# Optimization experiments

Measured on AMD Instinct MI355X. Metric: run time of the kernel, lower is better.

Reference implementation:

```python
import jax, jax.numpy as jnp
import numpy as np

EMBED = 256
HEADS = 8
SR = 2
RED = 2


def setup_inputs() -> dict:
    key = jax.random.key(0)
    ks = jax.random.split(key, 12)
    N, B, C = 1024, 64, EMBED
    inp = {
        "query": jax.random.normal(ks[0], (N, B, C), jnp.float32),
        "H": 32,
        "W": 32,
        "key": jax.random.normal(ks[1], (N, B, C), jnp.float32),
        "value": jax.random.normal(ks[2], (N, B, C), jnp.float32),
        # parameters
        "in_proj_weight": jax.random.normal(ks[3], (3 * C, C), jnp.float32) * (1.0 / np.sqrt(C)),
        "in_proj_bias": jnp.zeros((3 * C,), jnp.float32),
        "sr_w": jax.random.normal(ks[4], (C, C, SR, SR), jnp.float32) * np.sqrt(2.0 / (SR * SR * C)),
        "sr_b": jnp.zeros((C,), jnp.float32),
        "norm_g": jnp.ones((C,), jnp.float32),
        "norm_b": jnp.zeros((C,), jnp.float32),
        "out_w": jax.random.normal(ks[5], (C, C), jnp.float32) * (1.0 / np.sqrt(C)),
        "out_b": jnp.zeros((C,), jnp.float32),
        "se_w1": jax.random.normal(ks[6], (C // RED, C), jnp.float32) * 0.02,
        "se_w2": jax.random.normal(ks[7], (C, C // RED), jnp.float32) * 0.02,
    }
    return inp


def _angles(H, W):
    # get_index: a = (pi/2)*(i//W)/H, b = (pi/2)*(i%W)/W for flattened row-major index
    c = np.pi / 2
    idx = jnp.arange(H * W)
    a = c * (idx // W).astype(jnp.float32) / H
    b = c * (idx % W).astype(jnp.float32) / W
    return a, b


def _layernorm(x, g, b, eps=1e-5):
    mu = jnp.mean(x, -1, keepdims=True)
    var = jnp.mean(jnp.square(x - mu), -1, keepdims=True)
    return (x - mu) * jax.lax.rsqrt(var + eps) * g + b


def _abs_clamp(t, lo=1e-4, hi=1e4):
    return jnp.clip(jnp.abs(t), lo, hi) * jnp.sign(t)


def reference(query, H, W, key, value, in_proj_weight, in_proj_bias, sr_w, sr_b,
              norm_g, norm_b, out_w, out_b, se_w1, se_w2):
    N, B, C = query.shape
    h = HEADS
    hd = C // h
    scaling = hd ** (-0.5)

    x = jnp.transpose(query, (1, 0, 2))  # (B, N, C)

    # squeeze-excite gate from query: mean over tokens -> fc1 -> relu -> fc2 -> sigmoid
    se = jnp.mean(x, axis=1)                       # (B, C)
    se = jax.nn.sigmoid(jax.nn.relu(se @ se_w1.T) @ se_w2.T)  # (B, C)

    # spatial reduction conv (kernel=stride=sr_ratio) + layernorm for k/v source
    x_img = jnp.transpose(x, (0, 2, 1)).reshape(B, C, H, W)
    xr = jax.lax.conv_general_dilated(
        x_img, sr_w, window_strides=(SR, SR), padding="VALID",
        dimension_numbers=("NCHW", "OIHW", "NCHW"))
    xr = xr + sr_b[None, :, None, None]
    Hs, Ws = H // SR, W // SR
    Ns = Hs * Ws
    xr = jnp.transpose(xr.reshape(B, C, Ns), (0, 2, 1))  # (B, Ns, C)
    xr = _layernorm(xr, norm_g, norm_b)

    Wq, Wk, Wv = in_proj_weight[:C], in_proj_weight[C:2 * C], in_proj_weight[2 * C:]
    bq, bk, bv = in_proj_bias[:C], in_proj_bias[C:2 * C], in_proj_bias[2 * C:]

    def split_heads(t):  # (B, L, C) -> (B*h, L, hd)
        Bb, L, _ = t.shape
        return jnp.transpose(t.reshape(Bb, L, h, hd), (0, 2, 1, 3)).reshape(Bb * h, L, hd)

    q = split_heads((x @ Wq.T + bq) * scaling)
    k = split_heads(xr @ Wk.T + bk)
    v = split_heads(xr @ Wv.T + bv)

    q = jax.nn.relu(q)
    k = jax.nn.relu(k)

    # cosFormer-2d "sum" reweighting: cos(a_i - a_j) + cos(b_i - b_j)
    a, b = _angles(H, W)       # (N,)
    a2, b2 = _angles(Hs, Ws)   # (Ns,)

    def reweight(t, aa, bb):  # (BH, L, hd), angles (L,) -> (BH, L, 4*hd)
        aa = aa[None, :, None]
        bb = bb[None, :, None]
        return jnp.concatenate(
            [t * jnp.cos(aa), t * jnp.sin(aa), t * jnp.cos(bb), t * jnp.sin(bb)], axis=-1)

    q_ = reweight(q, a, b)     # (BH, N, 4hd)
    k_ = reweight(k, a2, b2)   # (BH, Ns, 4hd)

    # linear attention: never materialize the NxNs matrix
    kv = jnp.einsum("bnd,bnm->bdm", k_, v)             # (BH, 4hd, hd)
    denom = jnp.einsum("bnd,bd->bn", q_, k_.sum(1))    # (BH, N)
    denom = _abs_clamp(denom)
    attn = jnp.einsum("bnd,bdm->bnm", q_, kv) / denom[..., None]  # (BH, N, hd)

    attn = jnp.transpose(attn.reshape(B, h, N, hd), (0, 2, 1, 3)).reshape(B, N, C)
    out = attn @ out_w.T + out_b            # (B, N, C)
    out = out * se[:, None, :]              # SE channel gating
    return jnp.transpose(out, (1, 0, 2))    # (N, B, C)
```

## Files before the change

kernel.cpp:

```cpp
#include <hip/hip_runtime.h>

#define NTOK 1024
#define NB   64
#define CD   256
#define NHEAD 8
#define HDIM 32
#define NS 256
#define NBC 16384

typedef __attribute__((ext_vector_type(8))) short short8v;
typedef __attribute__((ext_vector_type(4))) short short4v;
typedef __attribute__((ext_vector_type(4))) float f32x4;

__device__ __forceinline__ unsigned bfr(float x){
  unsigned u = __float_as_uint(x);
  return (u + 0x7fffu + ((u>>16)&1u)) >> 16;
}
__device__ __forceinline__ void split2(float x, short &h, short &l){
  unsigned hu = bfr(x);
  float hf = __uint_as_float(hu << 16);
  unsigned lu = bfr(x - hf);
  h = (short)hu; l = (short)lu;
}

__global__ __launch_bounds__(256) void k_wcvt(const float* __restrict__ ipw, const float* __restrict__ ow,
                                              const float* __restrict__ srw,
                                              short* __restrict__ Wih, short* __restrict__ Wil,
                                              short* __restrict__ Woh, short* __restrict__ Wol,
                                              short* __restrict__ Wsh, short* __restrict__ Wsl){
  int u = blockIdx.x*256 + threadIdx.x;
  float xs[8];
  short* dh; short* dl; int dof;
  if (u < 24576){
    int n = u >> 5, off = (u & 31)*8;
    const float* s = ipw + n*CD + off;
    #pragma unroll
    for (int i=0;i<8;++i) xs[i] = s[i];
    dh = Wih; dl = Wil; dof = n*CD + off;
  } else if (u < 32768){
    int v = u - 24576;
    int n = v >> 5, off = (v & 31)*8;
    const float* s = ow + n*CD + off;
    #pragma unroll
    for (int i=0;i<8;++i) xs[i] = s[i];
    dh = Woh; dl = Wol; dof = n*CD + off;
  } else {
    int v = u - 32768;
    int n = v >> 7, koff = (v & 127)*8;
    int g = koff >> 8, cin0 = koff & 255;
    #pragma unroll
    for (int i=0;i<8;++i) xs[i] = srw[n*1024 + (cin0+i)*4 + g];
    dh = Wsh; dl = Wsl; dof = n*1024 + koff;
  }
  short8v h, l;
  #pragma unroll
  for (int i=0;i<8;++i){ short a,b; split2(xs[i],a,b); h[i]=a; l[i]=b; }
  *(short8v*)(dh + dof) = h;
  *(short8v*)(dl + dof) = l;
}

__global__ __launch_bounds__(256) void k_qcvt(const float* __restrict__ q, short* __restrict__ Qh,
                                              short* __restrict__ Ql){
  int idx = blockIdx.x*256 + threadIdx.x;
  int m = idx >> 5;
  int off = (idx & 31)*8;
  const float* src = q + (m & 1023)*NBC + (m >> 10)*CD + off;
  float4 a = *(const float4*)src;
  float4 b4 = *(const float4*)(src+4);
  float xs[8] = {a.x,a.y,a.z,a.w,b4.x,b4.y,b4.z,b4.w};
  short8v h, l;
  #pragma unroll
  for (int i=0;i<8;++i){ short hh,ll; split2(xs[i],hh,ll); h[i]=hh; l[i]=ll; }
  *(short8v*)(Qh + m*CD + off) = h;
  *(short8v*)(Ql + m*CD + off) = l;
}

__global__ __launch_bounds__(256) void k_trig(float* __restrict__ t1, float* __restrict__ t2){
  int n = blockIdx.x*256 + threadIdx.x;
  const float c = 1.57079632679489662f;
  float aa = c * (float)(n >> 5) / 32.0f;
  float bb = c * (float)(n & 31) / 32.0f;
  t1[n*4+0]=cosf(aa); t1[n*4+1]=sinf(aa); t1[n*4+2]=cosf(bb); t1[n*4+3]=sinf(bb);
  if (n < 256){
    float a2 = c * (float)(n >> 4) / 16.0f;
    float b2 = c * (float)(n & 15) / 16.0f;
    t2[n*4+0]=cosf(a2); t2[n*4+1]=sinf(a2); t2[n*4+2]=cosf(b2); t2[n*4+3]=sinf(b2);
  }
}

__global__ __launch_bounds__(256) void k_semean(const float* __restrict__ q, float* __restrict__ part){
  int b = blockIdx.x >> 2, qr = blockIdx.x & 3;
  int c = threadIdx.x;
  const float* qp = q + (qr*256)*NBC + b*CD + c;
  float s0=0.f,s1=0.f,s2=0.f,s3=0.f;
  for (int n=0;n<256;n+=4){
    s0 += qp[(n  )*NBC];
    s1 += qp[(n+1)*NBC];
    s2 += qp[(n+2)*NBC];
    s3 += qp[(n+3)*NBC];
  }
  part[blockIdx.x*256 + c] = (s0+s1)+(s2+s3);
}

__global__ __launch_bounds__(256) void k_semlp(const float* __restrict__ part, const float* __restrict__ w1,
                                               const float* __restrict__ w2, float* __restrict__ se){
  __shared__ float sm[256];
  __shared__ float s1s[128];
  int b = blockIdx.x, t = threadIdx.x;
  float s = (part[(b*4+0)*256+t]+part[(b*4+1)*256+t])+(part[(b*4+2)*256+t]+part[(b*4+3)*256+t]);
  sm[t] = s*(1.0f/1024.0f);
  __syncthreads();
  if (t < 128){
    float a = 0.f;
    const float* wr = w1 + t*256;
    for (int c=0;c<256;c+=4){
      float4 wf = *(const float4*)(wr+c);
      a += sm[c]*wf.x + sm[c+1]*wf.y + sm[c+2]*wf.z + sm[c+3]*wf.w;
    }
    s1s[t] = fmaxf(a, 0.f);
  }
  __syncthreads();
  float a = 0.f;
  const float* wr2 = w2 + t*128;
  for (int c=0;c<128;c+=4){
    float4 wf = *(const float4*)(wr2+c);
    a += s1s[c]*wf.x + s1s[c+1]*wf.y + s1s[c+2]*wf.z + s1s[c+3]*wf.w;
  }
  se[b*256+t] = 1.0f/(1.0f+expf(-a));
}

__global__ __launch_bounds__(256) void k_conv(const short* __restrict__ Qh, const short* __restrict__ Ql,
                                              const short* __restrict__ Wsh, const short* __restrict__ Wsl,
                                              const float* __restrict__ srb, float* __restrict__ xr){
  __shared__ __align__(16) short Ah[64*32];
  __shared__ __align__(16) short Al[64*32];
  __shared__ __align__(16) short Bh[128*32];
  __shared__ __align__(16) short Bl[128*32];
  int mblk = blockIdx.x >> 1, nblk = blockIdx.x & 1;
  int m0 = mblk*64, n0 = nblk*128;
  int b = mblk >> 2;
  int pos0 = m0 & 255;
  int t = threadIdx.x, wave = t>>6, lane = t&63;
  int wm = wave>>1, wn = wave&1;
  int q = lane>>4, r = lane&15;
  int ra = t>>2, pa = (t&3)*8;
  int posA = pos0 + ra, hs = posA>>4, ws2 = posA&15;
  const f32x4 fz = {0.f,0.f,0.f,0.f};
  f32x4 acc[2][4];
  #pragma unroll
  for (int s=0;s<2;++s)
    #pragma unroll
    for (int tt=0;tt<4;++tt) acc[s][tt] = fz;
  for (int kc=0; kc<32; ++kc){
    int g = kc>>3, cin0 = (kc&7)*32;
    int gh = g>>1, gw = g&1;
    int tok = (2*hs+gh)*32 + 2*ws2 + gw;
    int ga = ((b<<10) + tok)*CD + cin0 + pa;
    *(short8v*)(Ah + ra*32 + pa) = *(const short8v*)(Qh + ga);
    *(short8v*)(Al + ra*32 + pa) = *(const short8v*)(Ql + ga);
    int ko = kc*32;
    #pragma unroll
    for (int rep=0; rep<2; ++rep){
      int rr = ra + rep*64;
      int gb = (n0 + rr)*1024 + ko + pa;
      *(short8v*)(Bh + rr*32 + pa) = *(const short8v*)(Wsh + gb);
      *(short8v*)(Bl + rr*32 + pa) = *(const short8v*)(Wsl + gb);
    }
    __syncthreads();
    short8v ah[2], al[2];
    #pragma unroll
    for (int s=0;s<2;++s){
      int row = wm*32 + s*16 + r;
      ah[s] = *(const short8v*)(Ah + row*32 + q*8);
      al[s] = *(const short8v*)(Al + row*32 + q*8);
    }
    #pragma unroll
    for (int tt=0;tt<4;++tt){
      int brow = wn*64 + tt*16 + r;
      short8v bh = *(const short8v*)(Bh + brow*32 + q*8);
      short8v bl = *(const short8v*)(Bl + brow*32 + q*8);
      #pragma unroll
      for (int s=0;s<2;++s){
        acc[s][tt] = __builtin_amdgcn_mfma_f32_16x16x32_bf16(ah[s], bh, acc[s][tt], 0,0,0);
        acc[s][tt] = __builtin_amdgcn_mfma_f32_16x16x32_bf16(ah[s], bl, acc[s][tt], 0,0,0);
        acc[s][tt] = __builtin_amdgcn_mfma_f32_16x16x32_bf16(al[s], bh, acc[s][tt], 0,0,0);
      }
    }
    __syncthreads();
  }
  #pragma unroll
  for (int s=0;s<2;++s){
    #pragma unroll
    for (int tt=0;tt<4;++tt){
      int c = n0 + wn*64 + tt*16 + r;
      float bias = srb[c];
      #pragma unroll
      for (int i=0;i<4;++i){
        int m = m0 + wm*32 + s*16 + q*4 + i;
        xr[m*CD + c] = acc[s][tt][i] + bias;
      }
    }
  }
}

__global__ __launch_bounds__(256) void k_ln(const float* __restrict__ xr, const float* __restrict__ g,
                                            const float* __restrict__ bta, short* __restrict__ Xh,
                                            short* __restrict__ Xl){
  int wv = threadIdx.x >> 6, lane = threadIdx.x & 63;
  int row = blockIdx.x*4 + wv;
  float4 v = ((const float4*)(xr + row*CD))[lane];
  float s = (v.x+v.y)+(v.z+v.w);
  #pragma unroll
  for (int off=1; off<64; off<<=1) s += __shfl_xor(s, off, 64);
  float mu = s * (1.0f/256.0f);
  float dx=v.x-mu, dy=v.y-mu, dz=v.z-mu, dw=v.w-mu;
  float s2 = (dx*dx+dy*dy)+(dz*dz+dw*dw);
  #pragma unroll
  for (int off=1; off<64; off<<=1) s2 += __shfl_xor(s2, off, 64);
  float inv = 1.0f / sqrtf(s2*(1.0f/256.0f) + 1e-5f);
  float4 gr = ((const float4*)g)[lane];
  float4 br = ((const float4*)bta)[lane];
  float o0 = dx*inv*gr.x + br.x;
  float o1 = dy*inv*gr.y + br.y;
  float o2 = dz*inv*gr.z + br.z;
  float o3 = dw*inv*gr.w + br.w;
  short4v h, l; short a0,b0;
  split2(o0,a0,b0); h[0]=a0; l[0]=b0;
  split2(o1,a0,b0); h[1]=a0; l[1]=b0;
  split2(o2,a0,b0); h[2]=a0; l[2]=b0;
  split2(o3,a0,b0); h[3]=a0; l[3]=b0;
  *(short4v*)(Xh + row*CD + lane*4) = h;
  *(short4v*)(Xl + row*CD + lane*4) = l;
}

__global__ __launch_bounds__(256) void k_qproj(const short* __restrict__ Qh, const short* __restrict__ Ql,
                                               const short* __restrict__ Wih, const short* __restrict__ Wil,
                                               const float* __restrict__ ipb,
                                               short* __restrict__ Qbh, short* __restrict__ Qbl){
  __shared__ __align__(16) short smem[16384];
  short* Ah = smem;
  short* Al = smem + 4096;
  short* Bh = smem + 8192;
  short* Bl = smem + 12288;
  int mblk = blockIdx.x >> 1, nblk = blockIdx.x & 1;
  int m0 = mblk*128, n0 = nblk*128;
  int t = threadIdx.x, wave = t>>6, lane = t&63;
  int wm = wave>>1, wn = wave&1;
  int q = lane>>4, r = lane&15;
  int cr = t>>2, cp = (t&3)*8;
  int cpS = (((t&3) ^ ((cr>>1)&3)))*8;
  int sw8 = ((r>>1)&3)*8;
  const f32x4 fz = {0.f,0.f,0.f,0.f};
  f32x4 acc[4][4];
  #pragma unroll
  for (int s=0;s<4;++s)
    #pragma unroll
    for (int tt=0;tt<4;++tt) acc[s][tt] = fz;
  for (int kc=0; kc<8; ++kc){
    int ko = kc*32;
    #pragma unroll
    for (int rep=0; rep<2; ++rep){
      int rr = cr + rep*64;
      int ga = (m0 + rr)*CD + ko + cp;
      *(short8v*)(Ah + rr*32 + cpS) = *(const short8v*)(Qh + ga);
      *(short8v*)(Al + rr*32 + cpS) = *(const short8v*)(Ql + ga);
      int gb = (n0 + rr)*CD + ko + cp;
      *(short8v*)(Bh + rr*32 + cpS) = *(const short8v*)(Wih + gb);
      *(short8v*)(Bl + rr*32 + cpS) = *(const short8v*)(Wil + gb);
    }
    __syncthreads();
    short8v ah[4], al[4];
    #pragma unroll
    for (int s=0;s<4;++s){
      int row = wm*64 + s*16 + r;
      ah[s] = *(const short8v*)(Ah + row*32 + ((q*8)^sw8));
      al[s] = *(const short8v*)(Al + row*32 + ((q*8)^sw8));
    }
    #pragma unroll
    for (int tt=0;tt<4;++tt){
      int brow = wn*64 + tt*16 + r;
      short8v bh = *(const short8v*)(Bh + brow*32 + ((q*8)^sw8));
      short8v bl = *(const short8v*)(Bl + brow*32 + ((q*8)^sw8));
      #pragma unroll
      for (int s=0;s<4;++s){
        acc[s][tt] = __builtin_amdgcn_mfma_f32_16x16x32_bf16(ah[s], bh, acc[s][tt], 0,0,0);
        acc[s][tt] = __builtin_amdgcn_mfma_f32_16x16x32_bf16(ah[s], bl, acc[s][tt], 0,0,0);
        acc[s][tt] = __builtin_amdgcn_mfma_f32_16x16x32_bf16(al[s], bh, acc[s][tt], 0,0,0);
      }
    }
    __syncthreads();
  }
  const float sc = 0.17677669529663687f;
  short* T = smem;
  #pragma unroll
  for (int s=0;s<4;++s){
    #pragma unroll
    for (int tt=0;tt<4;++tt){
      int c_loc = wn*64 + tt*16 + r;
      int chunk = c_loc >> 3, cb = c_loc & 7;
      float bias = ipb[n0 + c_loc];
      #pragma unroll
      for (int i=0;i<4;++i){
        int m_loc = wm*64 + s*16 + q*4 + i;
        float val = fmaxf(acc[s][tt][i] + bias, 0.f)*sc;
        unsigned hu = bfr(val);
        T[m_loc*128 + ((chunk ^ (m_loc&7))<<3) + cb] = (short)hu;
        acc[s][tt][i] = val - __uint_as_float(hu<<16);
      }
    }
  }
  __syncthreads();
  {
    int mrl = (lane>>2);
    int ccl = lane&3;
    #pragma unroll
    for (int e=0;e<8;++e){
      int hl = e&3, mg = e>>2;
      int m_loc = wave*32 + mg*16 + mrl;
      int cc16 = hl*4 + ccl;
      short8v v = *(const short8v*)(T + m_loc*128 + ((cc16 ^ (m_loc&7))<<3));
      *(short8v*)(Qbh + ((size_t)((n0>>5)+hl))*2097152 + (size_t)(m0+m_loc)*32 + ccl*8) = v;
    }
  }
  __syncthreads();
  #pragma unroll
  for (int s=0;s<4;++s){
    #pragma unroll
    for (int tt=0;tt<4;++tt){
      int c_loc = wn*64 + tt*16 + r;
      int chunk = c_loc >> 3, cb = c_loc & 7;
      #pragma unroll
      for (int i=0;i<4;++i){
        int m_loc = wm*64 + s*16 + q*4 + i;
        T[m_loc*128 + ((chunk ^ (m_loc&7))<<3) + cb] = (short)bfr(acc[s][tt][i]);
      }
    }
  }
  __syncthreads();
  {
    int mrl = (lane>>2);
    int ccl = lane&3;
    #pragma unroll
    for (int e=0;e<8;++e){
      int hl = e&3, mg = e>>2;
      int m_loc = wave*32 + mg*16 + mrl;
      int cc16 = hl*4 + ccl;
      short8v v = *(const short8v*)(T + m_loc*128 + ((cc16 ^ (m_loc&7))<<3));
      *(short8v*)(Qbl + ((size_t)((n0>>5)+hl))*2097152 + (size_t)(m0+m_loc)*32 + ccl*8) = v;
    }
  }
}

__global__ __launch_bounds__(256) void k_kvproj(const short* __restrict__ Xh, const short* __restrict__ Xl,
                                                const short* __restrict__ Wkh, const short* __restrict__ Wkl,
                                                const float* __restrict__ ipb, float* __restrict__ kb,
                                                float* __restrict__ vb){
  __shared__ __align__(16) short Ah[128*32];
  __shared__ __align__(16) short Al[128*32];
  __shared__ __align__(16) short Bh[128*32];
  __shared__ __align__(16) short Bl[128*32];
  int mblk = blockIdx.x >> 2, nblk = blockIdx.x & 3;
  int m0 = mblk*128, n0 = nblk*128;
  int t = threadIdx.x, wave = t>>6, lane = t&63;
  int wm = wave>>1, wn = wave&1;
  int q = lane>>4, r = lane&15;
  int cr = t>>2, cp = (t&3)*8;
  const f32x4 fz = {0.f,0.f,0.f,0.f};
  f32x4 acc[4][4];
  #pragma unroll
  for (int s=0;s<4;++s)
    #pragma unroll
    for (int tt=0;tt<4;++tt) acc[s][tt] = fz;
  for (int kc=0; kc<8; ++kc){
    int ko = kc*32;
    #pragma unroll
    for (int rep=0; rep<2; ++rep){
      int rr = cr + rep*64;
      int ga = (m0 + rr)*CD + ko + cp;
      *(short8v*)(Ah + rr*32 + cp) = *(const short8v*)(Xh + ga);
      *(short8v*)(Al + rr*32 + cp) = *(const short8v*)(Xl + ga);
      int gb = (n0 + rr)*CD + ko + cp;
      *(short8v*)(Bh + rr*32 + cp) = *(const short8v*)(Wkh + gb);
      *(short8v*)(Bl + rr*32 + cp) = *(const short8v*)(Wkl + gb);
    }
    __syncthreads();
    short8v ah[4], al[4];
    #pragma unroll
    for (int s=0;s<4;++s){
      int row = wm*64 + s*16 + r;
      ah[s] = *(const short8v*)(Ah + row*32 + q*8);
      al[s] = *(const short8v*)(Al + row*32 + q*8);
    }
    #pragma unroll
    for (int tt=0;tt<4;++tt){
      int brow = wn*64 + tt*16 + r;
      short8v bh = *(const short8v*)(Bh + brow*32 + q*8);
      short8v bl = *(const short8v*)(Bl + brow*32 + q*8);
      #pragma unroll
      for (int s=0;s<4;++s){
        acc[s][tt] = __builtin_amdgcn_mfma_f32_16x16x32_bf16(ah[s], bh, acc[s][tt], 0,0,0);
        acc[s][tt] = __builtin_amdgcn_mfma_f32_16x16x32_bf16(ah[s], bl, acc[s][tt], 0,0,0);
        acc[s][tt] = __builtin_amdgcn_mfma_f32_16x16x32_bf16(al[s], bh, acc[s][tt], 0,0,0);
      }
    }
    __syncthreads();
  }
  #pragma unroll
  for (int s=0;s<4;++s){
    #pragma unroll
    for (int tt=0;tt<4;++tt){
      int c = n0 + wn*64 + tt*16 + r;
      float bias = ipb[256 + c];
      #pragma unroll
      for (int i=0;i<4;++i){
        int m = m0 + wm*64 + s*16 + q*4 + i;
        float v = acc[s][tt][i] + bias;
        if (c < 256) kb[m*CD + c] = fmaxf(v, 0.f);
        else         vb[m*CD + (c-256)] = v;
      }
    }
  }
}

__global__ __launch_bounds__(256) void k_kv(const float* __restrict__ kb, const float* __restrict__ vbuf,
                                            const float* __restrict__ t2, short* __restrict__ Bhp,
                                            short* __restrict__ Blp){
  int bh = blockIdx.x; int b = bh >> 3, h = bh & 7;
  int t = threadIdx.x; int jq = t >> 5, m = t & 31;
  float acc[4][4];
  #pragma unroll
  for (int p=0;p<4;++p){ acc[p][0]=0.f; acc[p][1]=0.f; acc[p][2]=0.f; acc[p][3]=0.f; }
  const float* kbase = kb + h*HDIM + jq*4;
  const float* vbase = vbuf + h*HDIM + m;
  for (int n=0;n<256;++n){
    int ro = (b*NS + n)*CD;
    float4 k4 = *(const float4*)(kbase + ro);
    float vv = vbase[ro];
    float4 tt = *(const float4*)(t2 + n*4);
    float tv[4] = {tt.x, tt.y, tt.z, tt.w};
    float kk[4] = {k4.x, k4.y, k4.z, k4.w};
    #pragma unroll
    for (int p=0;p<4;++p){
      float tp = tv[p]*vv;
      #pragma unroll
      for (int jj=0;jj<4;++jj) acc[p][jj] += tp*kk[jj];
    }
  }
  short* bhb = Bhp + bh*4608;
  short* blb = Blp + bh*4608;
  #pragma unroll
  for (int p=0;p<4;++p){
    short4v h4, l4;
    #pragma unroll
    for (int jj=0;jj<4;++jj){ short a,bq; split2(acc[p][jj],a,bq); h4[jj]=a; l4[jj]=bq; }
    *(short4v*)(bhb + (p*32+m)*32 + jq*4) = h4;
    *(short4v*)(blb + (p*32+m)*32 + jq*4) = l4;
  }
  if (t < 128){
    int p = t >> 5, j = t & 31;
    float s=0.f;
    const float* kp = kb + h*HDIM + j;
    for (int n=0;n<256;++n) s += t2[n*4+p]*kp[(b*NS+n)*CD];
    short a,bq; split2(s,a,bq);
    bhb[(128+p)*32 + j] = a;
    blb[(128+p)*32 + j] = bq;
  } else {
    int idx = t - 128;
    #pragma unroll
    for (int ii=0;ii<3;++ii){
      bhb[4224 + idx*3 + ii] = 0;
      blb[4224 + idx*3 + ii] = 0;
    }
  }
}

__global__ __launch_bounds__(256) void k_attn(const short* __restrict__ Qbh, const short* __restrict__ Qbl,
                                              const short* __restrict__ Bhg, const short* __restrict__ Blg,
                                              const float* __restrict__ t1,
                                              short* __restrict__ Ath, short* __restrict__ Atl){
  __shared__ __align__(16) short Bh[144*32];
  __shared__ __align__(16) short Bl[144*32];
  __shared__ __align__(16) short Ah[256*32];
  __shared__ __align__(16) short Al[256*32];
  int bh = blockIdx.x, b = bh>>3, h = bh&7;
  int t = threadIdx.x, lane = t&63, wave = t>>6;
  int q = lane>>4, r = lane&15;
  {
    const short8v* sh = (const short8v*)(Bhg + bh*4608);
    const short8v* sl = (const short8v*)(Blg + bh*4608);
    for (int i=t; i<576; i+=256){
      ((short8v*)Bh)[i] = sh[i];
      ((short8v*)Bl)[i] = sl[i];
    }
  }
  __syncthreads();
  short8v bf_h[9], bf_l[9];
  #pragma unroll
  for (int nt=0; nt<9; ++nt){
    int row = nt*16 + r;
    bf_h[nt] = *(const short8v*)(Bh + row*32 + q*8);
    bf_l[nt] = *(const short8v*)(Bl + row*32 + q*8);
  }
  const short* qh_base = Qbh + ((size_t)h*65536 + (size_t)b*1024)*32;
  const short* ql_base = Qbl + ((size_t)h*65536 + (size_t)b*1024)*32;
  const f32x4 fz = {0.f,0.f,0.f,0.f};
  for (int u=0; u<4; ++u){
    __syncthreads();
    {
      const short8v* sh = (const short8v*)(qh_base + (u*256 + t)*32);
      const short8v* sl = (const short8v*)(ql_base + (u*256 + t)*32);
      short8v* dh = (short8v*)(Ah + t*32);
      short8v* dl = (short8v*)(Al + t*32);
      #pragma unroll
      for (int i=0;i<4;++i){ dh[i]=sh[i]; dl[i]=sl[i]; }
    }
    __syncthreads();
    #pragma unroll
    for (int mi=0; mi<4; ++mi){
      int mt = wave*4 + mi;
      short8v ah = *(const short8v*)(Ah + (mt*16 + r)*32 + q*8);
      short8v al = *(const short8v*)(Al + (mt*16 + r)*32 + q*8);
      f32x4 acc[9];
      #pragma unroll
      for (int nt=0;nt<9;++nt) acc[nt]=fz;
      #pragma unroll
      for (int nt=0;nt<9;++nt){
        acc[nt] = __builtin_amdgcn_mfma_f32_16x16x32_bf16(ah, bf_h[nt], acc[nt],0,0,0);
        acc[nt] = __builtin_amdgcn_mfma_f32_16x16x32_bf16(ah, bf_l[nt], acc[nt],0,0,0);
        acc[nt] = __builtin_amdgcn_mfma_f32_16x16x32_bf16(al, bf_h[nt], acc[nt],0,0,0);
      }
      int nbase = u*256 + mt*16 + q*4;
      int src = lane & 48;
      #pragma unroll
      for (int i=0;i<4;++i){
        int n = nbase + i;
        float4 tv = *(const float4*)(t1 + n*4);
        float dp0 = __shfl(acc[8][i], src+0, 64);
        float dp1 = __shfl(acc[8][i], src+1, 64);
        float dp2 = __shfl(acc[8][i], src+2, 64);
        float dp3 = __shfl(acc[8][i], src+3, 64);
        float den = tv.x*dp0 + tv.y*dp1 + tv.z*dp2 + tv.w*dp3;
        float a0 = tv.x*acc[0][i] + tv.y*acc[2][i] + tv.z*acc[4][i] + tv.w*acc[6][i];
        float a1 = tv.x*acc[1][i] + tv.y*acc[3][i] + tv.z*acc[5][i] + tv.w*acc[7][i];
        float sgn = (den>0.f) ? 1.f : ((den<0.f)? -1.f : 0.f);
        float ad = fminf(fmaxf(fabsf(den), 1e-4f), 1e4f);
        float inv = (den != 0.f) ? 1.0f/(ad*sgn) : 0.f;
        float o0 = a0*inv, o1 = a1*inv;
        int mrow = b*NTOK + n;
        short h0,l0,h1,l1;
        split2(o0,h0,l0); split2(o1,h1,l1);
        Ath[mrow*CD + h*HDIM + r]      = h0;
        Atl[mrow*CD + h*HDIM + r]      = l0;
        Ath[mrow*CD + h*HDIM + 16 + r] = h1;
        Atl[mrow*CD + h*HDIM + 16 + r] = l1;
      }
    }
  }
}

__global__ __launch_bounds__(256) void k_outproj(const short* __restrict__ Ath, const short* __restrict__ Atl,
                                                 const short* __restrict__ Woh, const short* __restrict__ Wol,
                                                 const float* __restrict__ obv, const float* __restrict__ se,
                                                 float* __restrict__ dout){
  __shared__ __align__(16) short Ah[128*32];
  __shared__ __align__(16) short Al[128*32];
  __shared__ __align__(16) short Bh[128*32];
  __shared__ __align__(16) short Bl[128*32];
  int mblk = blockIdx.x >> 1, nblk = blockIdx.x & 1;
  int m0 = mblk*128, n0 = nblk*128;
  int t = threadIdx.x, wave = t>>6, lane = t&63;
  int wm = wave>>1, wn = wave&1;
  int q = lane>>4, r = lane&15;
  int cr = t>>2, cp = (t&3)*8;
  const f32x4 fz = {0.f,0.f,0.f,0.f};
  f32x4 acc[4][4];
  #pragma unroll
  for (int s=0;s<4;++s)
    #pragma unroll
    for (int tt=0;tt<4;++tt) acc[s][tt] = fz;
  for (int kc=0; kc<8; ++kc){
    int ko = kc*32;
    #pragma unroll
    for (int rep=0; rep<2; ++rep){
      int rr = cr + rep*64;
      int ga = (m0 + rr)*CD + ko + cp;
      *(short8v*)(Ah + rr*32 + cp) = *(const short8v*)(Ath + ga);
      *(short8v*)(Al + rr*32 + cp) = *(const short8v*)(Atl + ga);
      int gb = (n0 + rr)*CD + ko + cp;
      *(short8v*)(Bh + rr*32 + cp) = *(const short8v*)(Woh + gb);
      *(short8v*)(Bl + rr*32 + cp) = *(const short8v*)(Wol + gb);
    }
    __syncthreads();
    short8v ah[4], al[4];
    #pragma unroll
    for (int s=0;s<4;++s){
      int row = wm*64 + s*16 + r;
      ah[s] = *(const short8v*)(Ah + row*32 + q*8);
      al[s] = *(const short8v*)(Al + row*32 + q*8);
    }
    #pragma unroll
    for (int tt=0;tt<4;++tt){
      int brow = wn*64 + tt*16 + r;
      short8v bh = *(const short8v*)(Bh + brow*32 + q*8);
      short8v bl = *(const short8v*)(Bl + brow*32 + q*8);
      #pragma unroll
      for (int s=0;s<4;++s){
        acc[s][tt] = __builtin_amdgcn_mfma_f32_16x16x32_bf16(ah[s], bh, acc[s][tt], 0,0,0);
        acc[s][tt] = __builtin_amdgcn_mfma_f32_16x16x32_bf16(ah[s], bl, acc[s][tt], 0,0,0);
        acc[s][tt] = __builtin_amdgcn_mfma_f32_16x16x32_bf16(al[s], bh, acc[s][tt], 0,0,0);
      }
    }
    __syncthreads();
  }
  #pragma unroll
  for (int s=0;s<4;++s){
    #pragma unroll
    for (int tt=0;tt<4;++tt){
      int c = n0 + wn*64 + tt*16 + r;
      float bias = obv[c];
      #pragma unroll
      for (int i=0;i<4;++i){
        int m = m0 + wm*64 + s*16 + q*4 + i;
        int bb = m >> 10, ntok = m & 1023;
        float sev = se[bb*CD + c];
        dout[(ntok*NB + bb)*CD + c] = (acc[s][tt][i] + bias)*sev;
      }
    }
  }
}

extern "C" void kernel_launch(void* const* d_in, const int* in_sizes, int n_in,
                              void* d_out, int out_size, void* d_ws, size_t ws_size,
                              hipStream_t stream) {
  const float* query = (const float*)d_in[0];
  const float* ipw = (const float*)d_in[5];
  const float* ipb = (const float*)d_in[6];
  const float* srw = (const float*)d_in[7];
  const float* srb = (const float*)d_in[8];
  const float* ng  = (const float*)d_in[9];
  const float* nbb = (const float*)d_in[10];
  const float* ow  = (const float*)d_in[11];
  const float* obv = (const float*)d_in[12];
  const float* sw1 = (const float*)d_in[13];
  const float* sw2 = (const float*)d_in[14];
  float* dout = (float*)d_out;
  float* ws = (float*)d_ws;

  short* Qbh  = (short*)ws;
  short* Qbl  = (short*)(ws + 8388608);
  float* R1   = ws + 16777216;
  short* Qh   = (short*)R1;
  short* Ql   = (short*)(R1 + 8388608);
  float* kb   = R1;
  float* vb   = R1 + 4194304;
  short* Ath  = (short*)R1;
  short* Atl  = (short*)(R1 + 8388608);
  float* xr   = ws + 33554432;
  short* Xh   = (short*)(ws + 37748736);
  short* Xl   = (short*)(ws + 39845888);
  short* kvbh = (short*)(ws + 41943040);
  short* kvbl = (short*)(ws + 43122688);
  float* part = ws + 44302336;
  float* se   = ws + 44367872;
  float* t1   = ws + 44384256;
  float* t2   = ws + 44388352;
  short* Wih  = (short*)(ws + 44389376);
  short* Wil  = (short*)(ws + 44487680);
  short* Woh  = (short*)(ws + 44585984);
  short* Wol  = (short*)(ws + 44618752);
  short* Wsh  = (short*)(ws + 44651520);
  short* Wsl  = (short*)(ws + 44782592);

  k_wcvt  <<<256,  256,0,stream>>>(ipw, ow, srw, Wih, Wil, Woh, Wol, Wsh, Wsl);
  k_qcvt  <<<8192, 256,0,stream>>>(query, Qh, Ql);
  k_trig  <<<4,    256,0,stream>>>(t1, t2);
  k_semean<<<256,  256,0,stream>>>(query, part);
  k_semlp <<<64,   256,0,stream>>>(part, sw1, sw2, se);
  k_conv  <<<512,  256,0,stream>>>(Qh, Ql, Wsh, Wsl, srb, xr);
  k_ln    <<<4096, 256,0,stream>>>(xr, ng, nbb, Xh, Xl);
  k_qproj <<<1024, 256,0,stream>>>(Qh, Ql, Wih, Wil, ipb, Qbh, Qbl);
  k_kvproj<<<512,  256,0,stream>>>(Xh, Xl, Wih + 256*CD, Wil + 256*CD, ipb, kb, vb);
  k_kv    <<<512,  256,0,stream>>>(kb, vb, t2, kvbh, kvbl);
  k_attn  <<<512,  256,0,stream>>>(Qbh, Qbl, kvbh, kvbl, t1, Ath, Atl);
  k_outproj<<<1024,256,0,stream>>>(Ath, Atl, Woh, Wol, obv, se, dout);
}
```

Before: 457.7 us.

## Double-buffer GEMM tiles via direct global-to-LDS loads with swizzle

Replaces the register-staged global-to-shared tile loads in the conv, q/kv projection and output projection GEMMs with global_load_lds direct copies into a double-buffered, XOR-swizzled LDS layout. The next K-chunk is prefetched while MFMAs run on the current one, and one barrier per iteration is dropped. The SE mean now reads the transposed bf16 hi/lo query copy with contiguous vector loads instead of strided fp32 reads. This doubles LDS per block, which may reduce occupancy, and the async LDS writes rely on the barrier for correctness.

```diff
diff --git a/kernel.cpp b/kernel.cpp
--- a/kernel.cpp
+++ b/kernel.cpp
@@ -21,6 +21,11 @@
   float hf = __uint_as_float(hu << 16);
   unsigned lu = bfr(x - hf);
   h = (short)hu; l = (short)lu;
+}
+
+__device__ __forceinline__ void gl16(const void* g, void* l){
+  __builtin_amdgcn_global_load_lds((__attribute__((address_space(1))) void*)g,
+                                   (__attribute__((address_space(3))) void*)l, 16, 0, 0);
 }
 
 __global__ __launch_bounds__(256) void k_wcvt(const float* __restrict__ ipw, const float* __restrict__ ow,
@@ -88,18 +93,32 @@
   }
 }
 
-__global__ __launch_bounds__(256) void k_semean(const float* __restrict__ q, float* __restrict__ part){
+__global__ __launch_bounds__(256) void k_semean(const short* __restrict__ Qh, const short* __restrict__ Ql,
+                                                float* __restrict__ part){
+  __shared__ float red[8][256];
   int b = blockIdx.x >> 2, qr = blockIdx.x & 3;
-  int c = threadIdx.x;
-  const float* qp = q + (qr*256)*NBC + b*CD + c;
-  float s0=0.f,s1=0.f,s2=0.f,s3=0.f;
-  for (int n=0;n<256;n+=4){
-    s0 += qp[(n  )*NBC];
-    s1 += qp[(n+1)*NBC];
-    s2 += qp[(n+2)*NBC];
-    s3 += qp[(n+3)*NBC];
-  }
-  part[blockIdx.x*256 + c] = (s0+s1)+(s2+s3);
+  int t = threadIdx.x;
+  int c8 = (t & 31)*8;
+  int ng = t >> 5;
+  size_t base = ((size_t)(b*1024 + qr*256 + ng*32))*CD + c8;
+  float s[8] = {0.f,0.f,0.f,0.f,0.f,0.f,0.f,0.f};
+  for (int n=0;n<32;++n){
+    short8v vh = *(const short8v*)(Qh + base + (size_t)n*CD);
+    short8v vl = *(const short8v*)(Ql + base + (size_t)n*CD);
+    #pragma unroll
+    for (int j=0;j<8;++j){
+      float fh = __uint_as_float(((unsigned)(unsigned short)vh[j])<<16);
+      float fl = __uint_as_float(((unsigned)(unsigned short)vl[j])<<16);
+      s[j] += fh + fl;
+    }
+  }
+  #pragma unroll
+  for (int j=0;j<8;++j) red[ng][c8+j] = s[j];
+  __syncthreads();
+  float tot = 0.f;
+  #pragma unroll
+  for (int g=0;g<8;++g) tot += red[g][t];
+  part[blockIdx.x*256 + t] = tot;
 }
 
 __global__ __launch_bounds__(256) void k_semlp(const float* __restrict__ part, const float* __restrict__ w1,
@@ -132,10 +151,7 @@
 __global__ __launch_bounds__(256) void k_conv(const short* __restrict__ Qh, const short* __restrict__ Ql,
                                               const short* __restrict__ Wsh, const short* __restrict__ Wsl,
                                               const float* __restrict__ srb, float* __restrict__ xr){
-  __shared__ __align__(16) short Ah[64*32];
-  __shared__ __align__(16) short Al[64*32];
-  __shared__ __align__(16) short Bh[128*32];
-  __shared__ __align__(16) short Bl[128*32];
+  __shared__ __align__(16) short smem[24576];
   int mblk = blockIdx.x >> 1, nblk = blockIdx.x & 1;
   int m0 = mblk*64, n0 = nblk*128;
   int b = mblk >> 2;
@@ -143,42 +159,55 @@
   int t = threadIdx.x, wave = t>>6, lane = t&63;
   int wm = wave>>1, wn = wave&1;
   int q = lane>>4, r = lane&15;
-  int ra = t>>2, pa = (t&3)*8;
-  int posA = pos0 + ra, hs = posA>>4, ws2 = posA&15;
+  int lr = lane>>2;
+  int sx = (lane>>3)&3;
+  int lc = ((lane&3) ^ sx)*8;
+  int sw8 = ((r>>1)&3)*8;
   const f32x4 fz = {0.f,0.f,0.f,0.f};
   f32x4 acc[2][4];
   #pragma unroll
   for (int s=0;s<2;++s)
     #pragma unroll
     for (int tt=0;tt<4;++tt) acc[s][tt] = fz;
-  for (int kc=0; kc<32; ++kc){
+
+  auto stage = [&](int cur, int kc){
+    short* sb = smem + cur*12288;
+    short* wb = sb + wave*512;
     int g = kc>>3, cin0 = (kc&7)*32;
     int gh = g>>1, gw = g&1;
+    int ra = wave*16 + lr;
+    int posA = pos0 + ra, hs = posA>>4, ws2 = posA&15;
     int tok = (2*hs+gh)*32 + 2*ws2 + gw;
-    int ga = ((b<<10) + tok)*CD + cin0 + pa;
-    *(short8v*)(Ah + ra*32 + pa) = *(const short8v*)(Qh + ga);
-    *(short8v*)(Al + ra*32 + pa) = *(const short8v*)(Ql + ga);
+    size_t ga = ((size_t)((b<<10) + tok))*CD + cin0 + lc;
+    gl16(Qh + ga, wb);
+    gl16(Ql + ga, wb + 2048);
     int ko = kc*32;
     #pragma unroll
     for (int rep=0; rep<2; ++rep){
-      int rr = ra + rep*64;
-      int gb = (n0 + rr)*1024 + ko + pa;
-      *(short8v*)(Bh + rr*32 + pa) = *(const short8v*)(Wsh + gb);
-      *(short8v*)(Bl + rr*32 + pa) = *(const short8v*)(Wsl + gb);
-    }
-    __syncthreads();
+      int rb = ra + rep*64;
+      gl16(Wsh + (size_t)(n0+rb)*1024 + ko + lc, wb + 4096 + rep*2048);
+      gl16(Wsl + (size_t)(n0+rb)*1024 + ko + lc, wb + 8192 + rep*2048);
+    }
+  };
+
+  stage(0, 0);
+  __syncthreads();
+  int cur = 0;
+  for (int kc=0; kc<32; ++kc){
+    if (kc < 31) stage(cur^1, kc+1);
+    const short* sb = smem + cur*12288;
     short8v ah[2], al[2];
     #pragma unroll
     for (int s=0;s<2;++s){
       int row = wm*32 + s*16 + r;
-      ah[s] = *(const short8v*)(Ah + row*32 + q*8);
-      al[s] = *(const short8v*)(Al + row*32 + q*8);
+      ah[s] = *(const short8v*)(sb + row*32 + ((q*8)^sw8));
+      al[s] = *(const short8v*)(sb + 2048 + row*32 + ((q*8)^sw8));
     }
     #pragma unroll
     for (int tt=0;tt<4;++tt){
       int brow = wn*64 + tt*16 + r;
-      short8v bh = *(const short8v*)(Bh + brow*32 + q*8);
-      short8v bl = *(const short8v*)(Bl + brow*32 + q*8);
+      short8v bh = *(const short8v*)(sb + 4096 + brow*32 + ((q*8)^sw8));
+      short8v bl = *(const short8v*)(sb + 8192 + brow*32 + ((q*8)^sw8));
       #pragma unroll
       for (int s=0;s<2;++s){
         acc[s][tt] = __builtin_amdgcn_mfma_f32_16x16x32_bf16(ah[s], bh, acc[s][tt], 0,0,0);
@@ -187,6 +216,7 @@
       }
     }
     __syncthreads();
+    cur ^= 1;
   }
   #pragma unroll
   for (int s=0;s<2;++s){
@@ -237,18 +267,15 @@
                                                const short* __restrict__ Wih, const short* __restrict__ Wil,
                                                const float* __restrict__ ipb,
                                                short* __restrict__ Qbh, short* __restrict__ Qbl){
-  __shared__ __align__(16) short smem[16384];
-  short* Ah = smem;
-  short* Al = smem + 4096;
-  short* Bh = smem + 8192;
-  short* Bl = smem + 12288;
+  __shared__ __align__(16) short smem[32768];
   int mblk = blockIdx.x >> 1, nblk = blockIdx.x & 1;
   int m0 = mblk*128, n0 = nblk*128;
   int t = threadIdx.x, wave = t>>6, lane = t&63;
   int wm = wave>>1, wn = wave&1;
   int q = lane>>4, r = lane&15;
-  int cr = t>>2, cp = (t&3)*8;
-  int cpS = (((t&3) ^ ((cr>>1)&3)))*8;
+  int lr = lane>>2;
+  int sx = (lane>>3)&3;
+  int lc = ((lane&3) ^ sx)*8;
   int sw8 = ((r>>1)&3)*8;
   const f32x4 fz = {0.f,0.f,0.f,0.f};
   f32x4 acc[4][4];
@@ -256,31 +283,41 @@
   for (int s=0;s<4;++s)
     #pragma unroll
     for (int tt=0;tt<4;++tt) acc[s][tt] = fz;
+
+  auto stage = [&](int cur, int kc){
+    int ko = kc*32;
+    short* sb = smem + cur*16384;
+    short* wb = sb + wave*512;
+    #pragma unroll
+    for (int rep=0; rep<2; ++rep){
+      int ra = wave*16 + lr + rep*64;
+      size_t ga = (size_t)(m0+ra)*CD + ko + lc;
+      size_t gb = (size_t)(n0+ra)*CD + ko + lc;
+      gl16(Qh  + ga, wb + rep*2048);
+      gl16(Ql  + ga, wb + 4096  + rep*2048);
+      gl16(Wih + gb, wb + 8192  + rep*2048);
+      gl16(Wil + gb, wb + 12288 + rep*2048);
+    }
+  };
+
+  stage(0, 0);
+  __syncthreads();
+  int cur = 0;
   for (int kc=0; kc<8; ++kc){
-    int ko = kc*32;
-    #pragma unroll
-    for (int rep=0; rep<2; ++rep){
-      int rr = cr + rep*64;
-      int ga = (m0 + rr)*CD + ko + cp;
-      *(short8v*)(Ah + rr*32 + cpS) = *(const short8v*)(Qh + ga);
-      *(short8v*)(Al + rr*32 + cpS) = *(const short8v*)(Ql + ga);
-      int gb = (n0 + rr)*CD + ko + cp;
-      *(short8v*)(Bh + rr*32 + cpS) = *(const short8v*)(Wih + gb);
-      *(short8v*)(Bl + rr*32 + cpS) = *(const short8v*)(Wil + gb);
-    }
-    __syncthreads();
+    if (kc < 7) stage(cur^1, kc+1);
+    const short* sb = smem + cur*16384;
     short8v ah[4], al[4];
     #pragma unroll
     for (int s=0;s<4;++s){
       int row = wm*64 + s*16 + r;
-      ah[s] = *(const short8v*)(Ah + row*32 + ((q*8)^sw8));
-      al[s] = *(const short8v*)(Al + row*32 + ((q*8)^sw8));
+      ah[s] = *(const short8v*)(sb + row*32 + ((q*8)^sw8));
+      al[s] = *(const short8v*)(sb + 4096 + row*32 + ((q*8)^sw8));
     }
     #pragma unroll
     for (int tt=0;tt<4;++tt){
       int brow = wn*64 + tt*16 + r;
-      short8v bh = *(const short8v*)(Bh + brow*32 + ((q*8)^sw8));
-      short8v bl = *(const short8v*)(Bl + brow*32 + ((q*8)^sw8));
+      short8v bh = *(const short8v*)(sb + 8192 + brow*32 + ((q*8)^sw8));
+      short8v bl = *(const short8v*)(sb + 12288 + brow*32 + ((q*8)^sw8));
       #pragma unroll
       for (int s=0;s<4;++s){
         acc[s][tt] = __builtin_amdgcn_mfma_f32_16x16x32_bf16(ah[s], bh, acc[s][tt], 0,0,0);
@@ -289,6 +326,7 @@
       }
     }
     __syncthreads();
+    cur ^= 1;
   }
   const float sc = 0.17677669529663687f;
   short* T = smem;
@@ -355,47 +393,57 @@
                                                 const short* __restrict__ Wkh, const short* __restrict__ Wkl,
                                                 const float* __restrict__ ipb, float* __restrict__ kb,
                                                 float* __restrict__ vb){
-  __shared__ __align__(16) short Ah[128*32];
-  __shared__ __align__(16) short Al[128*32];
-  __shared__ __align__(16) short Bh[128*32];
-  __shared__ __align__(16) short Bl[128*32];
+  __shared__ __align__(16) short smem[32768];
   int mblk = blockIdx.x >> 2, nblk = blockIdx.x & 3;
   int m0 = mblk*128, n0 = nblk*128;
   int t = threadIdx.x, wave = t>>6, lane = t&63;
   int wm = wave>>1, wn = wave&1;
   int q = lane>>4, r = lane&15;
-  int cr = t>>2, cp = (t&3)*8;
+  int lr = lane>>2;
+  int sx = (lane>>3)&3;
+  int lc = ((lane&3) ^ sx)*8;
+  int sw8 = ((r>>1)&3)*8;
   const f32x4 fz = {0.f,0.f,0.f,0.f};
   f32x4 acc[4][4];
   #pragma unroll
   for (int s=0;s<4;++s)
     #pragma unroll
     for (int tt=0;tt<4;++tt) acc[s][tt] = fz;
+
+  auto stage = [&](int cur, int kc){
+    int ko = kc*32;
+    short* sb = smem + cur*16384;
+    short* wb = sb + wave*512;
+    #pragma unroll
+    for (int rep=0; rep<2; ++rep){
+      int ra = wave*16 + lr + rep*64;
+      size_t ga = (size_t)(m0+ra)*CD + ko + lc;
+      size_t gb = (size_t)(n0+ra)*CD + ko + lc;
+      gl16(Xh  + ga, wb + rep*2048);
+      gl16(Xl  + ga, wb + 4096  + rep*2048);
+      gl16(Wkh + gb, wb + 8192  + rep*2048);
+      gl16(Wkl + gb, wb + 12288 + rep*2048);
+    }
+  };
+
+  stage(0, 0);
+  __syncthreads();
+  int cur = 0;
   for (int kc=0; kc<8; ++kc){
-    int ko = kc*32;
-    #pragma unroll
-    for (int rep=0; rep<2; ++rep){
-      int rr = cr + rep*64;
-      int ga = (m0 + rr)*CD + ko + cp;
-      *(short8v*)(Ah + rr*32 + cp) = *(const short8v*)(Xh + ga);
-      *(short8v*)(Al + rr*32 + cp) = *(const short8v*)(Xl + ga);
-      int gb = (n0 + rr)*CD + ko + cp;
-      *(short8v*)(Bh + rr*32 + cp) = *(const short8v*)(Wkh + gb);
-      *(short8v*)(Bl + rr*32 + cp) = *(const short8v*)(Wkl + gb);
-    }
-    __syncthreads();
+    if (kc < 7) stage(cur^1, kc+1);
+    const short* sb = smem + cur*16384;
     short8v ah[4], al[4];
     #pragma unroll
     for (int s=0;s<4;++s){
       int row = wm*64 + s*16 + r;
-      ah[s] = *(const short8v*)(Ah + row*32 + q*8);
-      al[s] = *(const short8v*)(Al + row*32 + q*8);
+      ah[s] = *(const short8v*)(sb + row*32 + ((q*8)^sw8));
+      al[s] = *(const short8v*)(sb + 4096 + row*32 + ((q*8)^sw8));
     }
     #pragma unroll
     for (int tt=0;tt<4;++tt){
       int brow = wn*64 + tt*16 + r;
-      short8v bh = *(const short8v*)(Bh + brow*32 + q*8);
-      short8v bl = *(const short8v*)(Bl + brow*32 + q*8);
+      short8v bh = *(const short8v*)(sb + 8192 + brow*32 + ((q*8)^sw8));
+      short8v bl = *(const short8v*)(sb + 12288 + brow*32 + ((q*8)^sw8));
       #pragma unroll
       for (int s=0;s<4;++s){
         acc[s][tt] = __builtin_amdgcn_mfma_f32_16x16x32_bf16(ah[s], bh, acc[s][tt], 0,0,0);
@@ -404,6 +452,7 @@
       }
     }
     __syncthreads();
+    cur ^= 1;
   }
   #pragma unroll
   for (int s=0;s<4;++s){
@@ -562,47 +611,57 @@
                                                  const short* __restrict__ Woh, const short* __restrict__ Wol,
                                                  const float* __restrict__ obv, const float* __restrict__ se,
                                                  float* __restrict__ dout){
-  __shared__ __align__(16) short Ah[128*32];
-  __shared__ __align__(16) short Al[128*32];
-  __shared__ __align__(16) short Bh[128*32];
-  __shared__ __align__(16) short Bl[128*32];
+  __shared__ __align__(16) short smem[32768];
   int mblk = blockIdx.x >> 1, nblk = blockIdx.x & 1;
   int m0 = mblk*128, n0 = nblk*128;
   int t = threadIdx.x, wave = t>>6, lane = t&63;
   int wm = wave>>1, wn = wave&1;
   int q = lane>>4, r = lane&15;
-  int cr = t>>2, cp = (t&3)*8;
+  int lr = lane>>2;
+  int sx = (lane>>3)&3;
+  int lc = ((lane&3) ^ sx)*8;
+  int sw8 = ((r>>1)&3)*8;
   const f32x4 fz = {0.f,0.f,0.f,0.f};
   f32x4 acc[4][4];
   #pragma unroll
   for (int s=0;s<4;++s)
     #pragma unroll
     for (int tt=0;tt<4;++tt) acc[s][tt] = fz;
+
+  auto stage = [&](int cur, int kc){
+    int ko = kc*32;
+    short* sb = smem + cur*16384;
+    short* wb = sb + wave*512;
+    #pragma unroll
+    for (int rep=0; rep<2; ++rep){
+      int ra = wave*16 + lr + rep*64;
+      size_t ga = (size_t)(m0+ra)*CD + ko + lc;
+      size_t gb = (size_t)(n0+ra)*CD + ko + lc;
+      gl16(Ath + ga, wb + rep*2048);
+      gl16(Atl + ga, wb + 4096  + rep*2048);
+      gl16(Woh + gb, wb + 8192  + rep*2048);
+      gl16(Wol + gb, wb + 12288 + rep*2048);
+    }
+  };
+
+  stage(0, 0);
+  __syncthreads();
+  int cur = 0;
   for (int kc=0; kc<8; ++kc){
-    int ko = kc*32;
-    #pragma unroll
-    for (int rep=0; rep<2; ++rep){
-      int rr = cr + rep*64;
-      int ga = (m0 + rr)*CD + ko + cp;
-      *(short8v*)(Ah + rr*32 + cp) = *(const short8v*)(Ath + ga);
-      *(short8v*)(Al + rr*32 + cp) = *(const short8v*)(Atl + ga);
-      int gb = (n0 + rr)*CD + ko + cp;
-      *(short8v*)(Bh + rr*32 + cp) = *(const short8v*)(Woh + gb);
-      *(short8v*)(Bl + rr*32 + cp) = *(const short8v*)(Wol + gb);
-    }
-    __syncthreads();
+    if (kc < 7) stage(cur^1, kc+1);
+    const short* sb = smem + cur*16384;
     short8v ah[4], al[4];
     #pragma unroll
     for (int s=0;s<4;++s){
       int row = wm*64 + s*16 + r;
-      ah[s] = *(const short8v*)(Ah + row*32 + q*8);
-      al[s] = *(const short8v*)(Al + row*32 + q*8);
+      ah[s] = *(const short8v*)(sb + row*32 + ((q*8)^sw8));
+      al[s] = *(const short8v*)(sb + 4096 + row*32 + ((q*8)^sw8));
     }
     #pragma unroll
     for (int tt=0;tt<4;++tt){
       int brow = wn*64 + tt*16 + r;
-      short8v bh = *(const short8v*)(Bh + brow*32 + q*8);
-      short8v bl = *(const short8v*)(Bl + brow*32 + q*8);
+      short8v bh = *(const short8v*)(sb + 8192 + brow*32 + ((q*8)^sw8));
+      short8v bl = *(const short8v*)(sb + 12288 + brow*32 + ((q*8)^sw8));
       #pragma unroll
       for (int s=0;s<4;++s){
         acc[s][tt] = __builtin_amdgcn_mfma_f32_16x16x32_bf16(ah[s], bh, acc[s][tt], 0,0,0);
@@ -611,6 +670,7 @@
       }
     }
     __syncthreads();
+    cur ^= 1;
   }
   #pragma unroll
   for (int s=0;s<4;++s){
@@ -674,7 +734,7 @@
   k_wcvt  <<<256,  256,0,stream>>>(ipw, ow, srw, Wih, Wil, Woh, Wol, Wsh, Wsl);
   k_qcvt  <<<8192, 256,0,stream>>>(query, Qh, Ql);
   k_trig  <<<4,    256,0,stream>>>(t1, t2);
-  k_semean<<<256,  256,0,stream>>>(query, part);
+  k_semean<<<256,  256,0,stream>>>(Qh, Ql, part);
   k_semlp <<<64,   256,0,stream>>>(part, sw1, sw2, se);
   k_conv  <<<512,  256,0,stream>>>(Qh, Ql, Wsh, Wsl, srb, xr);
   k_ln    <<<4096, 256,0,stream>>>(xr, ng, nbb, Xh, Xl);
```

After: 465.6 us. No clear change (+1.7%).
